# Optimization experiments

Measured on AMD Instinct MI355X. Metric: run time of the kernel, lower is better.

## Reference

```python
import jax, jax.numpy as jnp
import numpy as np

B, S, D, H, E = 4, 2048, 512, 8, 4  # batch, seq, embed, heads, expand
HD = D // H


def setup_inputs() -> dict:
    key = jax.random.key(0)
    ks = jax.random.split(key, 9)
    s = lambda k, shape, fan: jax.random.normal(k, shape, jnp.float32) * (fan ** -0.5)
    return {
        "x": jax.random.normal(ks[0], (B, S, D), jnp.float32),
        "Wq": s(ks[1], (D, D), D),
        "Wk": s(ks[2], (D, D), D),
        "Wv": s(ks[3], (D, D), D),
        "Wo": s(ks[4], (D, D), D),
        "W1": s(ks[5], (D, D * E), D),
        "b1": jnp.zeros((D * E,), jnp.float32),
        "W2": s(ks[6], (D * E, D), D * E),
        "b2": jnp.zeros((D,), jnp.float32),
    }


def _encoder_layer(x, Wq, Wk, Wv, Wo, W1, b1, W2, b2):
    # NOTE: source computes InstanceNorm1d twice but discards both results -> no-ops.
    scale = D ** -0.25  # applied to BOTH q and k (net 1/sqrt(embed_dim))
    q = (x @ Wq).reshape(B, S, H, HD).transpose(0, 2, 1, 3) * scale  # [B,H,S,hd]
    k = (x @ Wk).reshape(B, S, H, HD).transpose(0, 2, 1, 3) * scale
    v = (x @ Wv).reshape(B, S, H, HD).transpose(0, 2, 1, 3)
    scores = jnp.einsum('bhqd,bhkd->bhqk', q, k)  # [B,H,S,S]
    attn = jax.nn.softmax(scores, axis=-1)
    o = jnp.einsum('bhqk,bhkd->bhqd', attn, v)  # [B,H,S,hd]
    o = o.transpose(0, 2, 1, 3).reshape(B, S, D)
    x = o @ Wo + x  # residual 1
    h = jax.nn.gelu(x @ W1 + b1, approximate=True)  # torch GELU(approximate='tanh')
    return h @ W2 + b2 + x  # residual 2 (dropout=0, eval)


def reference(x, Wq, Wk, Wv, Wo, W1, b1, W2, b2):
    return _encoder_layer(x, Wq, Wk, Wv, Wo, W1, b1, W2, b2)
```

## Files before the change

### kernel.cpp

```cpp
#include <hip/hip_runtime.h>
#include <hip/hip_bf16.h>


typedef __bf16 bf16;
typedef __attribute__((ext_vector_type(8))) __bf16 bf16x8;
typedef __attribute__((ext_vector_type(4))) __bf16 bf16x4;
typedef __attribute__((ext_vector_type(4))) float f32x4;
typedef __attribute__((ext_vector_type(16))) float f32x16;
typedef __attribute__((ext_vector_type(2))) unsigned int u32x2;
typedef __attribute__((ext_vector_type(4))) unsigned int u32x4;

#define LOG2E 1.4426950408889634f
#define SCORE_SCALE 0.044194173824159216f
#define SCALE_L2E (SCORE_SCALE * LOG2E)
#define FIXED_M 12.0f

#if __has_builtin(__builtin_amdgcn_exp2f)
#define EXP2(x) __builtin_amdgcn_exp2f(x)
#else
#define EXP2(x) exp2f(x)
#endif

__device__ __forceinline__ void gl_lds16(const bf16* g, bf16* l) {
  __builtin_amdgcn_global_load_lds(
      (const __attribute__((address_space(1))) unsigned int*)g,
      (__attribute__((address_space(3))) unsigned int*)l, 16, 0, 0);
}

template <int N>
__device__ __forceinline__ void wait_vm_barrier() {
  if constexpr (N == 0)
    asm volatile("s_waitcnt vmcnt(0)\ns_barrier" ::: "memory");
  else if constexpr (N == 3)
    asm volatile("s_waitcnt vmcnt(3)\ns_barrier" ::: "memory");
  else if constexpr (N == 4)
    asm volatile("s_waitcnt vmcnt(4)\ns_barrier" ::: "memory");
}

__device__ __forceinline__ float gelu_tanh(float x) {
  float u = 0.7978845608028654f * (x + 0.044715f * x * x * x);
  float e = EXP2(u * (2.0f * LOG2E));
  float th = 1.0f - 2.0f / (e + 1.0f);
  return 0.5f * x * (1.0f + th);
}

__device__ __forceinline__ f32x4 mfma_bf16(bf16x8 a, bf16x8 b, f32x4 c) {
  return __builtin_amdgcn_mfma_f32_16x16x32_bf16(a, b, c, 0, 0, 0);
}
__device__ __forceinline__ f32x16 mfma32x16(bf16x8 a, bf16x8 b, f32x16 c) {
  return __builtin_amdgcn_mfma_f32_32x32x16_bf16(a, b, c, 0, 0, 0);
}

__device__ __forceinline__ void plswap(unsigned int& a, unsigned int& b) {
  asm volatile("v_permlane32_swap_b32 %0, %1" : "+v"(a), "+v"(b));
}

template <int MODE, typename OutT, int TN>
__global__ __launch_bounds__(256, 2) void gemm_bt(
    const bf16* __restrict__ A, const bf16* __restrict__ Bt,
    OutT* __restrict__ C, const float* __restrict__ bias,
    const float* __restrict__ resf, const bf16* __restrict__ resb,
    bf16* __restrict__ vt, int M, int N, int K) {
  constexpr int MI = (TN == 128) ? 4 : 2;
  constexpr int NBUF = (TN == 128) ? 2 : 3;
  __shared__ __align__(16) bf16 sA[NBUF][128 * 32];
  __shared__ __align__(16) bf16 sB[NBUF][TN * 32];
  const int tid = threadIdx.x;
  const int lane = tid & 63;
  const int quad = lane >> 4, lc = lane & 15;
  const int wave = tid >> 6;
  const int wr = (TN == 128) ? (wave >> 1) : wave;
  const int wc = (TN == 128) ? (wave & 1) : 0;
  const int m0 = blockIdx.y * 128, n0 = blockIdx.x * TN;

  const int srow = tid >> 2;
  const int kc = (tid & 3) * 8;
  const bf16* Ag1 = A + (size_t)(m0 + srow) * K + kc;
  const bf16* Ag2 = A + (size_t)(m0 + 64 + srow) * K + kc;
  const bf16* Bg1 = Bt + (size_t)(n0 + srow) * K + kc;
  const bf16* Bg2 = Bt + (size_t)(n0 + 64 + srow) * K + kc;
  const int o1 = tid * 8, o2 = (tid + 256) * 8;

  f32x4 acc[MI][4];
#pragma unroll
  for (int mi = 0; mi < MI; ++mi)
#pragma unroll
    for (int ni = 0; ni < 4; ++ni) acc[mi][ni] = (f32x4){0.f, 0.f, 0.f, 0.f};

  const int kIters = K >> 5;

  if constexpr (TN == 128) {
    gl_lds16(Ag1, sA[0] + o1);
    gl_lds16(Ag2, sA[0] + o2);
    gl_lds16(Bg1, sB[0] + o1);
    gl_lds16(Bg2, sB[0] + o2);
    Ag1 += 32; Ag2 += 32; Bg1 += 32; Bg2 += 32;

    for (int kt = 0; kt < kIters; ++kt) {
      __syncthreads();
      const bf16* cA = sA[kt & 1];
      const bf16* cB = sB[kt & 1];
      if (kt + 1 < kIters) {
        bf16* nA = sA[(kt + 1) & 1];
        bf16* nB = sB[(kt + 1) & 1];
        gl_lds16(Ag1, nA + o1);
        gl_lds16(Ag2, nA + o2);
        gl_lds16(Bg1, nB + o1);
        gl_lds16(Bg2, nB + o2);
        Ag1 += 32; Ag2 += 32; Bg1 += 32; Bg2 += 32;
      }
      bf16x8 af[MI], bfm[4];
#pragma unroll
      for (int i = 0; i < MI; ++i)
        af[i] = *(const bf16x8*)(cA +
                                 ((wr * 64 + i * 16 + lc) * 32 + quad * 8));
#pragma unroll
      for (int i = 0; i < 4; ++i)
        bfm[i] =
            *(const bf16x8*)(cB + ((wc * 64 + i * 16 + lc) * 32 + quad * 8));
#pragma unroll
      for (int mi = 0; mi < MI; ++mi)
#pragma unroll
        for (int ni = 0; ni < 4; ++ni)
          acc[mi][ni] = mfma_bf16(af[mi], bfm[ni], acc[mi][ni]);
    }
  } else {
    auto stage = [&](int t) {
      bf16* a = sA[t % 3];
      bf16* bb = sB[t % 3];
      gl_lds16(Ag1 + t * 32, a + o1);
      gl_lds16(Ag2 + t * 32, a + o2);
      gl_lds16(Bg1 + t * 32, bb + o1);
    };
    stage(0);
    stage(1);
    for (int kt = 0; kt < kIters; ++kt) {
      if (kt + 1 < kIters)
        wait_vm_barrier<3>();
      else
        wait_vm_barrier<0>();
      if (kt + 2 < kIters) stage(kt + 2);
      const bf16* cA = sA[kt % 3];
      const bf16* cB = sB[kt % 3];
      bf16x8 af[MI], bfm[4];
#pragma unroll
      for (int i = 0; i < MI; ++i)
        af[i] = *(const bf16x8*)(cA +
                                 ((wr * 32 + i * 16 + lc) * 32 + quad * 8));
#pragma unroll
      for (int i = 0; i < 4; ++i)
        bfm[i] = *(const bf16x8*)(cB + ((i * 16 + lc) * 32 + quad * 8));
#pragma unroll
      for (int mi = 0; mi < MI; ++mi)
#pragma unroll
        for (int ni = 0; ni < 4; ++ni)
          acc[mi][ni] = mfma_bf16(af[mi], bfm[ni], acc[mi][ni]);
    }
  }

  if constexpr (MODE == 0) {
    if (n0 >= 1024) {
#pragma unroll
      for (int mi = 0; mi < MI; ++mi) {
        const int row0 = m0 + wr * (16 * MI) + mi * 16 + quad * 4;
        const int bb = row0 >> 11, s0 = row0 & 2047;
#pragma unroll
        for (int ni = 0; ni < 4; ++ni) {
          const int col = n0 + wc * 64 + ni * 16 + lc;
          const int hh = (col >> 6) & 7, d = col & 63;
          bf16x4 pb;
#pragma unroll
          for (int r = 0; r < 4; ++r) pb[r] = (bf16)acc[mi][ni][r];
          *(bf16x4*)(vt + ((size_t)((bb * 8 + hh) * 64 + d)) * 2048 + s0) = pb;
        }
      }
      return;
    }
  }
#pragma unroll
  for (int mi = 0; mi < MI; ++mi) {
#pragma unroll
    for (int r = 0; r < 4; ++r) {
      const int row = m0 + wr * (16 * MI) + mi * 16 + quad * 4 + r;
#pragma unroll
      for (int ni = 0; ni < 4; ++ni) {
        const int col = n0 + wc * 64 + ni * 16 + lc;
        const size_t idx = (size_t)row * N + col;
        float v = acc[mi][ni][r];
        if (MODE == 1) v += resf[idx];
        if (MODE == 2) v = gelu_tanh(v + bias[col]);
        if (MODE == 3) v += bias[col] + (float)resb[idx];
        C[idx] = (OutT)v;
      }
    }
  }
}

__global__ __launch_bounds__(256, 2) void flash_attn(
    const bf16* __restrict__ QKV, const bf16* __restrict__ Vt,
    bf16* __restrict__ O) {
  const int tid = threadIdx.x;
  const int lane = tid & 63, wave = tid >> 6;
  const int lo5 = lane & 31, hi = lane >> 5;
  const int lin = blockIdx.y * 16 + blockIdx.x;
  const int xcd = lin & 7, slot = lin >> 3;
  const int bh = xcd * 4 + (slot >> 4);
  const int qt = slot & 15;
  const int b = bh >> 3, h = bh & 7;
  const int q0 = qt * 128 + wave * 32;

  __shared__ __align__(16) bf16 sK[3][4096];
  __shared__ __align__(16) bf16 sV[3][4096];

  const bf16* Qrow = QKV + (size_t)(b * 2048 + q0 + lo5) * 1536 + h * 64;
  bf16x8 qf[4];
#pragma unroll
  for (int i = 0; i < 4; ++i) qf[i] = *(const bf16x8*)(Qrow + i * 16 + hi * 8);

  const int colsw = (((lane & 7) ^ (lane >> 3)) << 3);
  const bf16* Kg0 = QKV + (size_t)b * 2048 * 1536 + 512 + (size_t)h * 64 +
                    (size_t)(wave * 16 + (lane >> 3)) * 1536 + colsw;
  const bf16* Vg0 = Vt + (size_t)bh * 64 * 2048 +
                    (size_t)(wave * 16 + (lane >> 3)) * 2048 + colsw;
  const int stag = wave * 1024;
  const int m7 = lo5 & 7;

  f32x16 oacc[2];
  oacc[0] = (f32x16)(0.f);
  oacc[1] = (f32x16)(0.f);
  float rs0 = 0.f, rs1 = 0.f, rs2 = 0.f, rs3 = 0.f;

  auto stage = [&](int t) {
    bf16* dk = sK[t % 3] + stag;
    bf16* dv = sV[t % 3] + stag;
    gl_lds16(Kg0 + (size_t)t * 64 * 1536, dk);
    gl_lds16(Kg0 + (size_t)(t * 64 + 8) * 1536, dk + 512);
    gl_lds16(Vg0 + t * 64, dv);
    gl_lds16(Vg0 + t * 64 + 8 * 2048, dv + 512);
  };
  stage(0);
  stage(1);

  for (int kt = 0; kt < 32; ++kt) {
    if (kt == 31)
      wait_vm_barrier<0>();
    else
      wait_vm_barrier<4>();
    if (kt + 2 < 32) stage(kt + 2);
    const bf16* cK = sK[kt % 3];
    const bf16* cV = sV[kt % 3];

    bf16x8 vf[2][4];
#pragma unroll
    for (int dh = 0; dh < 2; ++dh) {
      const int Rd = dh * 32 + lo5;
#pragma unroll
      for (int w = 0; w < 4; ++w)
        vf[dh][w] =
            *(const bf16x8*)(cV + Rd * 64 + (((2 * w + hi) ^ m7) << 3));
    }

    bf16x8 paw[4];
#pragma unroll
    for (int hl = 0; hl < 2; ++hl) {
      f32x16 st = (f32x16)(0.f);
      const int R = hl * 32 + lo5;
      __builtin_amdgcn_s_setprio(1);
#pragma unroll
      for (int i = 0; i < 4; ++i) {
        bf16x8 kf =
            *(const bf16x8*)(cK + R * 64 + (((2 * i + hi) ^ m7) << 3));
        st = mfma32x16(kf, qf[i], st);
      }
      __builtin_amdgcn_s_setprio(0);
      unsigned int q32[4][2];
#pragma unroll
      for (int g = 0; g < 4; ++g) {
        bf16x4 pb;
        float p0 = EXP2(st[4 * g + 0] * SCALE_L2E - FIXED_M);
        float p1 = EXP2(st[4 * g + 1] * SCALE_L2E - FIXED_M);
        float p2 = EXP2(st[4 * g + 2] * SCALE_L2E - FIXED_M);
        float p3 = EXP2(st[4 * g + 3] * SCALE_L2E - FIXED_M);
        rs0 += p0; rs1 += p1; rs2 += p2; rs3 += p3;
        pb[0] = (bf16)p0; pb[1] = (bf16)p1; pb[2] = (bf16)p2; pb[3] = (bf16)p3;
        u32x2 w2 = __builtin_bit_cast(u32x2, pb);
        q32[g][0] = w2[0];
        q32[g][1] = w2[1];
      }
#pragma unroll
      for (int t = 0; t < 2; ++t) {
        unsigned int a0 = q32[2 * t][0], a1 = q32[2 * t][1];
        unsigned int b0 = q32[2 * t + 1][0], b1 = q32[2 * t + 1][1];
        plswap(a0, b0);
        plswap(a1, b1);
        u32x4 f = {a0, a1, b0, b1};
        paw[hl * 2 + t] = __builtin_bit_cast(bf16x8, f);
      }
    }

    __builtin_amdgcn_s_setprio(1);
#pragma unroll
    for (int dh = 0; dh < 2; ++dh)
#pragma unroll
      for (int w = 0; w < 4; ++w)
        oacc[dh] = mfma32x16(paw[w], vf[dh][w], oacc[dh]);
    __builtin_amdgcn_s_setprio(0);
  }

  float rsum = (rs0 + rs1) + (rs2 + rs3);
  rsum += __shfl_xor(rsum, 32, 64);
  const size_t obase = (size_t)(b * 2048 + q0) * 512 + h * 64;
#pragma unroll
  for (int r = 0; r < 16; ++r) {
    const int qloc = (r & 3) + 8 * (r >> 2) + 4 * hi;
    const float inv = 1.0f / __shfl(rsum, qloc, 64);
#pragma unroll
    for (int dh = 0; dh < 2; ++dh)
      O[obase + (size_t)qloc * 512 + dh * 32 + lo5] =
          (bf16)(oacc[dh][r] * inv);
  }
}

__global__ __launch_bounds__(256) void prep(
    const float* __restrict__ x, const float* __restrict__ Wq,
    const float* __restrict__ Wk, const float* __restrict__ Wv,
    const float* __restrict__ Wo, const float* __restrict__ W1,
    const float* __restrict__ W2, bf16* __restrict__ xb,
    bf16* __restrict__ WqkvT, bf16* __restrict__ WoT, bf16* __restrict__ W1T,
    bf16* __restrict__ W2T) {
  const int bid = blockIdx.x;
  if (bid < 4096) {
    const size_t i = ((size_t)bid * 256 + threadIdx.x) * 4;
    const float4 v = *(const float4*)(x + i);
    bf16x4 o;
    o[0] = (bf16)v.x; o[1] = (bf16)v.y; o[2] = (bf16)v.z; o[3] = (bf16)v.w;
    *(bf16x4*)(xb + i) = o;
    return;
  }
  const int t = bid - 4096;
  const float* in;
  bf16* out;
  int in_ld, out_ld, bx, by;
  if (t < 1024) {
    const int q = t >> 8, r = t & 255;
    bx = r & 15; by = r >> 4; in_ld = 512; out_ld = 512;
    in = (q == 0) ? Wq : (q == 1) ? Wk : (q == 2) ? Wv : Wo;
    out = (q == 0) ? WqkvT
          : (q == 1) ? WqkvT + 512 * 512
          : (q == 2) ? WqkvT + 2 * 512 * 512
                     : WoT;
  } else if (t < 2048) {
    const int r = t - 1024;
    bx = r & 63; by = r >> 6; in_ld = 2048; out_ld = 512;
    in = W1; out = W1T;
  } else {
    const int r = t - 2048;
    bx = r & 15; by = r >> 4; in_ld = 512; out_ld = 2048;
    in = W2; out = W2T;
  }
  __shared__ __align__(16) bf16 tl[32][33];
  const int tx = threadIdx.x & 31, ty = threadIdx.x >> 5;
  const int n0 = bx * 32, k0 = by * 32;
#pragma unroll
  for (int i = 0; i < 4; ++i)
    tl[ty + 8 * i][tx] = (bf16)in[(size_t)(k0 + ty + 8 * i) * in_ld + n0 + tx];
  __syncthreads();
#pragma unroll
  for (int i = 0; i < 4; ++i)
    out[(size_t)(n0 + ty + 8 * i) * out_ld + k0 + tx] = tl[tx][ty + 8 * i];
}

extern "C" void kernel_launch(void* const* d_in, const int* in_sizes, int n_in,
                              void* d_out, int out_size, void* d_ws,
                              size_t ws_size, hipStream_t stream) {
  const float* x = (const float*)d_in[0];
  const float* Wq = (const float*)d_in[1];
  const float* Wk = (const float*)d_in[2];
  const float* Wv = (const float*)d_in[3];
  const float* Wo = (const float*)d_in[4];
  const float* W1 = (const float*)d_in[5];
  const float* b1 = (const float*)d_in[6];
  const float* W2 = (const float*)d_in[7];
  const float* b2 = (const float*)d_in[8];
  float* out = (float*)d_out;

  char* ws = (char*)d_ws;
  size_t off = 0;
  auto alloc = [&](size_t bytes) {
    char* p = ws + off;
    off += (bytes + 255) & ~(size_t)255;
    return p;
  };
  bf16* WqkvT = (bf16*)alloc(1536ULL * 512 * 2);
  bf16* WoT = (bf16*)alloc(512ULL * 512 * 2);
  bf16* W1T = (bf16*)alloc(2048ULL * 512 * 2);
  bf16* W2T = (bf16*)alloc(512ULL * 2048 * 2);
  bf16* xb = (bf16*)alloc(8192ULL * 512 * 2);
  bf16* QKV = (bf16*)alloc(8192ULL * 1536 * 2);
  bf16* Vt = (bf16*)alloc(32ULL * 64 * 2048 * 2);
  bf16* attn = (bf16*)alloc(8192ULL * 512 * 2);
  bf16* x2 = xb;
  bf16* hbuf = QKV;

  const dim3 tb(256);
  prep<<<dim3(7168), tb, 0, stream>>>(x, Wq, Wk, Wv, Wo, W1, W2, xb, WqkvT,
                                      WoT, W1T, W2T);
  gemm_bt<0, bf16, 128><<<dim3(12, 64), tb, 0, stream>>>(
      xb, WqkvT, QKV, nullptr, nullptr, nullptr, Vt, 8192, 1536, 512);
  flash_attn<<<dim3(16, 32), tb, 0, stream>>>(QKV, Vt, attn);
  gemm_bt<1, bf16, 64><<<dim3(8, 64), tb, 0, stream>>>(
      attn, WoT, x2, nullptr, x, nullptr, nullptr, 8192, 512, 512);
  gemm_bt<2, bf16, 128><<<dim3(16, 64), tb, 0, stream>>>(
      x2, W1T, hbuf, b1, nullptr, nullptr, nullptr, 8192, 2048, 512);
  gemm_bt<3, float, 64><<<dim3(8, 64), tb, 0, stream>>>(
      hbuf, W2T, out, b2, nullptr, x2, nullptr, 8192, 512, 2048);
}
```

Before: 247.0 us.

## Add 256x256 tile GEMM for FFN1 and interleave softmax with PV MFMAs

Adds a new 512-thread GEMM kernel with 256x256 tiles and a 3-stage LDS pipeline for the W1+GELU projection, giving more data reuse per block than the 128-tile kernel. Separately, the attention loop now issues both QK^T score MFMA chains together, then interleaves the softmax of one half with the PV MFMAs of the other so exp work overlaps matrix work. The larger tile raises register and LDS pressure and launches only 256 blocks, which may lower occupancy on the device.

```diff
diff --git a/kernel.cpp b/kernel.cpp
--- a/kernel.cpp
+++ b/kernel.cpp
@@ -196,6 +196,84 @@
   }
 }
 
+__global__ __launch_bounds__(512, 2) void gemm256(
+    const bf16* __restrict__ A, const bf16* __restrict__ Bt,
+    bf16* __restrict__ C, const float* __restrict__ bias, int M, int N,
+    int K) {
+  __shared__ __align__(16) bf16 sA[3][256 * 32];
+  __shared__ __align__(16) bf16 sB[3][256 * 32];
+  const int tid = threadIdx.x;
+  const int lane = tid & 63;
+  const int quad = lane >> 4, lc = lane & 15;
+  const int w8 = tid >> 6;
+  const int wr = w8 >> 2, wc = w8 & 3;
+  const int m0 = blockIdx.y * 256, n0 = blockIdx.x * 256;
+
+  const int sr = lane >> 2;
+  const int sc = (lane & 3) * 8;
+
+  f32x4 acc[8][4];
+#pragma unroll
+  for (int mi = 0; mi < 8; ++mi)
+#pragma unroll
+    for (int ni = 0; ni < 4; ++ni) acc[mi][ni] = (f32x4){0.f, 0.f, 0.f, 0.f};
+
+  auto stage = [&](int t) {
+    const int k0 = t * 32;
+    bf16* a = sA[t % 3];
+    bf16* bb = sB[t % 3];
+#pragma unroll
+    for (int j = 0; j < 2; ++j) {
+      const int blk = w8 * 2 + j;
+      gl_lds16(A + (size_t)(m0 + blk * 16 + sr) * K + k0 + sc, a + blk * 512);
+      gl_lds16(Bt + (size_t)(n0 + blk * 16 + sr) * K + k0 + sc,
+               bb + blk * 512);
+    }
+  };
+
+  const int kIters = K >> 5;
+  stage(0);
+  stage(1);
+
+  for (int kt = 0; kt < kIters; ++kt) {
+    if (kt + 1 < kIters)
+      wait_vm_barrier<4>();
+    else
+      wait_vm_barrier<0>();
+    if (kt + 2 < kIters) stage(kt + 2);
+    const bf16* cA = sA[kt % 3];
+    const bf16* cB = sB[kt % 3];
+
+    bf16x8 af[8], bfm[4];
+#pragma unroll
+    for (int i = 0; i < 8; ++i)
+      af[i] =
+          *(const bf16x8*)(cA + ((wr * 128 + i * 16 + lc) * 32 + quad * 8));
+#pragma unroll
+    for (int i = 0; i < 4; ++i)
+      bfm[i] =
+          *(const bf16x8*)(cB + ((wc * 64 + i * 16 + lc) * 32 + quad * 8));
+#pragma unroll
+    for (int mi = 0; mi < 8; ++mi)
+#pragma unroll
+      for (int ni = 0; ni < 4; ++ni)
+        acc[mi][ni] = mfma_bf16(af[mi], bfm[ni], acc[mi][ni]);
+  }
+
+#pragma unroll
+  for (int mi = 0; mi < 8; ++mi) {
+#pragma unroll
+    for (int r = 0; r < 4; ++r) {
+      const int row = m0 + wr * 128 + mi * 16 + quad * 4 + r;
+#pragma unroll
+      for (int ni = 0; ni < 4; ++ni) {
+        const int col = n0 + wc * 64 + ni * 16 + lc;
+        C[(size_t)row * N + col] = (bf16)gelu_tanh(acc[mi][ni][r] + bias[col]);
+      }
+    }
+  }
+}
+
 __global__ __launch_bounds__(256, 2) void flash_attn(
     const bf16* __restrict__ QKV, const bf16* __restrict__ Vt,
     bf16* __restrict__ O) {
@@ -241,6 +319,34 @@
   stage(0);
   stage(1);
 
+  bf16x8 paw[4];
+
+  auto softmax = [&](const f32x16& st, int hl) {
+    unsigned int q32[4][2];
+#pragma unroll
+    for (int g = 0; g < 4; ++g) {
+      bf16x4 pb;
+      float p0 = EXP2(st[4 * g + 0] * SCALE_L2E - FIXED_M);
+      float p1 = EXP2(st[4 * g + 1] * SCALE_L2E - FIXED_M);
+      float p2 = EXP2(st[4 * g + 2] * SCALE_L2E - FIXED_M);
+      float p3 = EXP2(st[4 * g + 3] * SCALE_L2E - FIXED_M);
+      rs0 += p0; rs1 += p1; rs2 += p2; rs3 += p3;
+      pb[0] = (bf16)p0; pb[1] = (bf16)p1; pb[2] = (bf16)p2; pb[3] = (bf16)p3;
+      u32x2 w2 = __builtin_bit_cast(u32x2, pb);
+      q32[g][0] = w2[0];
+      q32[g][1] = w2[1];
+    }
+#pragma unroll
+    for (int t = 0; t < 2; ++t) {
+      unsigned int a0 = q32[2 * t][0], a1 = q32[2 * t][1];
+      unsigned int b0 = q32[2 * t + 1][0], b1 = q32[2 * t + 1][1];
+      plswap(a0, b0);
+      plswap(a1, b1);
+      u32x4 f = {a0, a1, b0, b1};
+      paw[hl * 2 + t] = __builtin_bit_cast(bf16x8, f);
+    }
+  };
+
   for (int kt = 0; kt < 32; ++kt) {
     if (kt == 31)
       wait_vm_barrier<0>();
@@ -250,7 +356,7 @@
     const bf16* cK = sK[kt % 3];
     const bf16* cV = sV[kt % 3];
 
-    bf16x8 vf[2][4];
+    bf16x8 vf[2][4], kf[2][4];
 #pragma unroll
     for (int dh = 0; dh < 2; ++dh) {
       const int Rd = dh * 32 + lo5;
@@ -259,51 +365,37 @@
         vf[dh][w] =
             *(const bf16x8*)(cV + Rd * 64 + (((2 * w + hi) ^ m7) << 3));
     }
-
-    bf16x8 paw[4];
 #pragma unroll
     for (int hl = 0; hl < 2; ++hl) {
-      f32x16 st = (f32x16)(0.f);
       const int R = hl * 32 + lo5;
-      __builtin_amdgcn_s_setprio(1);
-#pragma unroll
-      for (int i = 0; i < 4; ++i) {
-        bf16x8 kf =
+#pragma unroll
+      for (int i = 0; i < 4; ++i)
+        kf[hl][i] =
             *(const bf16x8*)(cK + R * 64 + (((2 * i + hi) ^ m7) << 3));
-        st = mfma32x16(kf, qf[i], st);
-      }
-      __builtin_amdgcn_s_setprio(0);
-      unsigned int q32[4][2];
-#pragma unroll
-      for (int g = 0; g < 4; ++g) {
-        bf16x4 pb;
-        float p0 = EXP2(st[4 * g + 0] * SCALE_L2E - FIXED_M);
-        float p1 = EXP2(st[4 * g + 1] * SCALE_L2E - FIXED_M);
-        float p2 = EXP2(st[4 * g + 2] * SCALE_L2E - FIXED_M);
-        float p3 = EXP2(st[4 * g + 3] * SCALE_L2E - FIXED_M);
-        rs0 += p0; rs1 += p1; rs2 += p2; rs3 += p3;
-        pb[0] = (bf16)p0; pb[1] = (bf16)p1; pb[2] = (bf16)p2; pb[3] = (bf16)p3;
-        u32x2 w2 = __builtin_bit_cast(u32x2, pb);
-        q32[g][0] = w2[0];
-        q32[g][1] = w2[1];
-      }
-#pragma unroll
-      for (int t = 0; t < 2; ++t) {
-        unsigned int a0 = q32[2 * t][0], a1 = q32[2 * t][1];
-        unsigned int b0 = q32[2 * t + 1][0], b1 = q32[2 * t + 1][1];
-        plswap(a0, b0);
-        plswap(a1, b1);
-        u32x4 f = {a0, a1, b0, b1};
-        paw[hl * 2 + t] = __builtin_bit_cast(bf16x8, f);
-      }
-    }
-
+    }
+
+    f32x16 st0 = (f32x16)(0.f), st1 = (f32x16)(0.f);
     __builtin_amdgcn_s_setprio(1);
 #pragma unroll
-    for (int dh = 0; dh < 2; ++dh)
-#pragma unroll
-      for (int w = 0; w < 4; ++w)
-        oacc[dh] = mfma32x16(paw[w], vf[dh][w], oacc[dh]);
+    for (int i = 0; i < 4; ++i) {
+      st0 = mfma32x16(kf[0][i], qf[i], st0);
+      st1 = mfma32x16(kf[1][i], qf[i], st1);
+    }
+    __builtin_amdgcn_s_setprio(0);
+
+    softmax(st0, 0);
+#pragma unroll
+    for (int w = 0; w < 2; ++w) {
+      oacc[0] = mfma32x16(paw[w], vf[0][w], oacc[0]);
+      oacc[1] = mfma32x16(paw[w], vf[1][w], oacc[1]);
+    }
+    softmax(st1, 1);
+    __builtin_amdgcn_s_setprio(1);
+#pragma unroll
+    for (int w = 2; w < 4; ++w) {
+      oacc[0] = mfma32x16(paw[w], vf[0][w], oacc[0]);
+      oacc[1] = mfma32x16(paw[w], vf[1][w], oacc[1]);
+    }
     __builtin_amdgcn_s_setprio(0);
   }
 
@@ -410,8 +502,8 @@
   flash_attn<<<dim3(16, 32), tb, 0, stream>>>(QKV, Vt, attn);
   gemm_bt<1, bf16, 64><<<dim3(8, 64), tb, 0, stream>>>(
       attn, WoT, x2, nullptr, x, nullptr, nullptr, 8192, 512, 512);
-  gemm_bt<2, bf16, 128><<<dim3(16, 64), tb, 0, stream>>>(
-      x2, W1T, hbuf, b1, nullptr, nullptr, nullptr, 8192, 2048, 512);
+  gemm256<<<dim3(8, 32), dim3(512), 0, stream>>>(x2, W1T, hbuf, b1, 8192,
+                                                 2048, 512);
   gemm_bt<3, float, 64><<<dim3(8, 64), tb, 0, stream>>>(
       hbuf, W2T, out, b2, nullptr, x2, nullptr, 8192, 512, 2048);
 }
```

After: 251.7 us. No clear change (+1.9%).
